# Kernel tuning notes

Hardware: AMD Instinct MI355X
Metric: run time of the kernel (lower is better)

The kernel has to match this reference:

```python
import jax, jax.numpy as jnp
import numpy as np

N_NODES = 10000
N_EDGES = 640000
DIM = 128


def setup_inputs() -> dict:
    key = jax.random.key(0)
    ks = jax.random.split(key, 10)
    s = 1.0 / np.sqrt(DIM)
    return {
        "x": jax.random.normal(ks[0], (N_NODES, DIM), dtype=jnp.float32),
        "edge_index": jax.random.randint(ks[1], (2, N_EDGES), 0, N_NODES, dtype=jnp.int64),
        "fc_w": jax.random.normal(ks[2], (DIM, DIM), dtype=jnp.float32) * s,
        "fc_b": jax.random.normal(ks[3], (DIM,), dtype=jnp.float32) * s,
        "f_lw": jax.random.normal(ks[4], (DIM, DIM), dtype=jnp.float32) * s,
        "f_lb": jax.random.normal(ks[5], (DIM,), dtype=jnp.float32) * s,
        "f_rw": jax.random.normal(ks[6], (DIM, DIM), dtype=jnp.float32) * s,
        "n_lw": jax.random.normal(ks[7], (DIM, DIM), dtype=jnp.float32) * s,
        "n_lb": jax.random.normal(ks[8], (DIM,), dtype=jnp.float32) * s,
        "n_rw": jax.random.normal(ks[9], (DIM, DIM), dtype=jnp.float32) * s,
    }


def _sage_conv(h, src, dst, lw, lb, rw, n_nodes):
    # mean aggregation of source-node features at target nodes
    msg = h[src]                                                   # [E, D]
    summed = jax.ops.segment_sum(msg, dst, num_segments=n_nodes)   # [N, D]
    cnt = jax.ops.segment_sum(jnp.ones_like(dst, dtype=h.dtype), dst, num_segments=n_nodes)
    agg = summed / jnp.maximum(cnt, 1.0)[:, None]
    # PyG SAGEConv: lin_l(agg) + lin_r(x); lin_l has bias, lin_r does not
    return agg @ lw.T + lb + h @ rw.T


def reference(x, edge_index, fc_w, fc_b, f_lw, f_lb, f_rw, n_lw, n_lb, n_rw):
    n_nodes = x.shape[0]
    src, dst = edge_index[0], edge_index[1]
    inp = x @ fc_w.T + fc_b                                        # fc residual branch
    h = jax.nn.relu(_sage_conv(x, src, dst, f_lw, f_lb, f_rw, n_nodes))
    # dropout(p=0.3) is identity in eval mode
    h = _sage_conv(h, src, dst, n_lw, n_lb, n_rw, n_nodes)
    return jax.nn.relu(h + inp)
```

## Files before the change

### kernel.cpp

```cpp
#include <hip/hip_runtime.h>

#define NN 10000
#define NE 640000
#define DIM 128
#define NB 157
#define REGCAP 4608
#define MT1 157
#define G_FILL 625
#define NODECAP 128

typedef __attribute__((ext_vector_type(8))) short bf16x8;
typedef __attribute__((ext_vector_type(4))) float f32x4;

__device__ __forceinline__ unsigned short f2bf(float f) {
    unsigned u = __float_as_uint(f);
    u += 0x7FFFu + ((u >> 16) & 1u);
    return (unsigned short)(u >> 16);
}
__device__ __forceinline__ float bf2f(unsigned short h) {
    return __uint_as_float(((unsigned)h) << 16);
}

__global__ __launch_bounds__(256) void prep_k(
        const float* __restrict__ w0, const float* __restrict__ w1,
        const float* __restrict__ w2, const float* __restrict__ w3,
        const float* __restrict__ w4,
        unsigned short* __restrict__ wb, int* __restrict__ gcur) {
    int t = blockIdx.x * 256 + threadIdx.x;
    if (t < NB) gcur[t] = t * REGCAP;
    int plane = t >> 14;
    int i = t & 16383;
    const float* wp = (plane == 0) ? w0 : (plane == 1) ? w1 :
                      (plane == 2) ? w2 : (plane == 3) ? w3 : w4;
    wb[t] = f2bf(wp[i]);
}

__global__ __launch_bounds__(256) void mega1_k(
        const float* __restrict__ A,
        const unsigned short* __restrict__ wb,
        unsigned short* __restrict__ xlb,
        float* __restrict__ xr, float* __restrict__ xc,
        const int* __restrict__ src, const int* __restrict__ dst,
        int* __restrict__ gcur, unsigned* __restrict__ region) {
    int b = blockIdx.x;
    int tid = threadIdx.x;
    if (b < G_FILL) {
        __shared__ int start[NB + 1];
        __shared__ int cur[NB];
        __shared__ int gbase[NB];
        __shared__ unsigned sorted[1024];
        if (tid < NB + 1) start[tid] = 0;
        __syncthreads();
        int e4 = b * 1024 + tid * 4;
        int4 s = *(const int4*)(src + e4);
        int4 d = *(const int4*)(dst + e4);
        unsigned p0 = ((unsigned)d.x << 16) | (unsigned)s.x;
        unsigned p1 = ((unsigned)d.y << 16) | (unsigned)s.y;
        unsigned p2 = ((unsigned)d.z << 16) | (unsigned)s.z;
        unsigned p3 = ((unsigned)d.w << 16) | (unsigned)s.w;
        int k0 = d.x >> 6, k1 = d.y >> 6, k2 = d.z >> 6, k3 = d.w >> 6;
        atomicAdd(&start[k0 + 1], 1);
        atomicAdd(&start[k1 + 1], 1);
        atomicAdd(&start[k2 + 1], 1);
        atomicAdd(&start[k3 + 1], 1);
        __syncthreads();
        for (int off = 1; off < NB + 1; off <<= 1) {
            int v = 0;
            if (tid <= NB && tid >= off) v = start[tid - off];
            __syncthreads();
            if (tid <= NB && tid >= off) start[tid] += v;
            __syncthreads();
        }
        if (tid < NB) cur[tid] = start[tid];
        __syncthreads();
        int q;
        q = atomicAdd(&cur[k0], 1); sorted[q] = p0;
        q = atomicAdd(&cur[k1], 1); sorted[q] = p1;
        q = atomicAdd(&cur[k2], 1); sorted[q] = p2;
        q = atomicAdd(&cur[k3], 1); sorted[q] = p3;
        __syncthreads();
        if (tid < NB) {
            int len = start[tid + 1] - start[tid];
            gbase[tid] = (len > 0) ? atomicAdd(&gcur[tid], len) : 0;
        }
        __syncthreads();
#pragma unroll
        for (int i = tid; i < 1024; i += 256) {
            unsigned e = sorted[i];
            int bb = (int)(e >> 16) >> 6;
            int gpos = gbase[bb] + (i - start[bb]);
            if (gpos < (bb + 1) * REGCAP) region[gpos] = e;
        }
        return;
    }
    int gb = b - G_FILL;
    int plane = gb / MT1;
    int mt = gb % MT1;
    const unsigned short* W = wb + (size_t)plane * (DIM * DIM);
    int lane = tid & 63;
    int wv = tid >> 6;
    int mr = lane & 15, q = lane >> 4;
    int m0 = mt * 64 + wv * 16;
    int mc = min(m0 + mr, NN - 1);

    bf16x8 afr[4];
#pragma unroll
    for (int kc = 0; kc < 4; ++kc) {
        const float* ap = A + (size_t)mc * DIM + kc * 32 + q * 8;
        float4 v0 = *(const float4*)ap;
        float4 v1 = *(const float4*)(ap + 4);
        bf16x8 f;
        f[0] = (short)f2bf(v0.x); f[1] = (short)f2bf(v0.y);
        f[2] = (short)f2bf(v0.z); f[3] = (short)f2bf(v0.w);
        f[4] = (short)f2bf(v1.x); f[5] = (short)f2bf(v1.y);
        f[6] = (short)f2bf(v1.z); f[7] = (short)f2bf(v1.w);
        afr[kc] = f;
    }
    f32x4 acc[8];
#pragma unroll
    for (int nt = 0; nt < 8; ++nt) acc[nt] = (f32x4){0.f, 0.f, 0.f, 0.f};
#pragma unroll
    for (int nt = 0; nt < 8; ++nt) {
        const unsigned short* wp = W + (size_t)(nt * 16 + mr) * DIM;
#pragma unroll
        for (int kc = 0; kc < 4; ++kc) {
            bf16x8 wfr = *(const bf16x8*)(const void*)(wp + kc * 32 + q * 8);
            acc[nt] = __builtin_amdgcn_mfma_f32_16x16x32_bf16(afr[kc], wfr, acc[nt], 0, 0, 0);
        }
    }
#pragma unroll
    for (int r = 0; r < 4; ++r) {
        int ms = m0 + q * 4 + r;
        if (ms >= NN) continue;
        if (plane == 0) {
#pragma unroll
            for (int nt = 0; nt < 8; ++nt)
                xlb[(size_t)ms * DIM + nt * 16 + mr] = f2bf(acc[nt][r]);
        } else {
            float* o = (plane == 1) ? xr : xc;
#pragma unroll
            for (int nt = 0; nt < 8; ++nt)
                o[(size_t)ms * DIM + nt * 16 + mr] = acc[nt][r];
        }
    }
}

template<int MODE>
__global__ __launch_bounds__(256) void agg_k(
        const unsigned short* __restrict__ gsrc,
        const float* __restrict__ xr, const float* __restrict__ b0v,
        const int* __restrict__ gcur, const unsigned* __restrict__ region,
        unsigned short* __restrict__ outb) {
    int blk = blockIdx.x;
    int b = blk >> 2, sub = blk & 3;
    int n0 = b * 64 + sub * 16;
    int tid = threadIdx.x;
    __shared__ unsigned short list[16][NODECAP];
    __shared__ int cnt[16];
    if (tid < 16) cnt[tid] = 0;
    __syncthreads();
    int R = min(gcur[b] - b * REGCAP, REGCAP);
    const unsigned* reg = region + (size_t)b * REGCAP;
    for (int i = tid; i < R; i += 256) {
        unsigned e = reg[i];
        int nl = (int)(e >> 16) - n0;
        if ((unsigned)nl < 16u) {
            int slot = atomicAdd(&cnt[nl], 1);
            if (slot < NODECAP) list[nl][slot] = (unsigned short)(e & 0xFFFFu);
        }
    }
    __syncthreads();

    int g = tid >> 4, d8 = tid & 15;
    int node = n0 + g;
    if (node >= NN) return;
    int deg = min(cnt[g], NODECAP);
    float a[8];
#pragma unroll
    for (int j = 0; j < 8; ++j) a[j] = 0.f;
    union U { int4 v; unsigned short us[8]; };
    int r = 0;
    for (; r + 4 <= deg; r += 4) {
        int i0 = list[g][r + 0];
        int i1 = list[g][r + 1];
        int i2 = list[g][r + 2];
        int i3 = list[g][r + 3];
        U u0, u1, u2, u3;
        u0.v = *(const int4*)(const void*)(gsrc + (size_t)i0 * DIM + d8 * 8);
        u1.v = *(const int4*)(const void*)(gsrc + (size_t)i1 * DIM + d8 * 8);
        u2.v = *(const int4*)(const void*)(gsrc + (size_t)i2 * DIM + d8 * 8);
        u3.v = *(const int4*)(const void*)(gsrc + (size_t)i3 * DIM + d8 * 8);
#pragma unroll
        for (int j = 0; j < 8; ++j)
            a[j] += bf2f(u0.us[j]) + bf2f(u1.us[j]) + bf2f(u2.us[j]) + bf2f(u3.us[j]);
    }
    for (; r < deg; ++r) {
        int i0 = list[g][r];
        U u0;
        u0.v = *(const int4*)(const void*)(gsrc + (size_t)i0 * DIM + d8 * 8);
#pragma unroll
        for (int j = 0; j < 8; ++j) a[j] += bf2f(u0.us[j]);
    }
    float inv = 1.f / fmaxf((float)deg, 1.f);
    U o;
    if (MODE == 0) {
        const float* xp = xr + (size_t)node * DIM + d8 * 8;
        float4 r0 = *(const float4*)xp;
        float4 r1 = *(const float4*)(xp + 4);
        const float* bp = b0v + d8 * 8;
        float4 c0 = *(const float4*)bp;
        float4 c1 = *(const float4*)(bp + 4);
        float rv[8] = {r0.x, r0.y, r0.z, r0.w, r1.x, r1.y, r1.z, r1.w};
        float bv[8] = {c0.x, c0.y, c0.z, c0.w, c1.x, c1.y, c1.z, c1.w};
#pragma unroll
        for (int j = 0; j < 8; ++j)
            o.us[j] = f2bf(fmaxf(a[j] * inv + rv[j] + bv[j], 0.f));
    } else {
#pragma unroll
        for (int j = 0; j < 8; ++j) o.us[j] = f2bf(a[j] * inv);
    }
    *(int4*)(void*)(outb + (size_t)node * DIM + d8 * 8) = o.v;
}

__global__ __launch_bounds__(256) void mega2_k(
        const unsigned short* __restrict__ m1b,
        const unsigned short* __restrict__ h1b,
        const unsigned short* __restrict__ wb,
        const float* __restrict__ xc,
        const float* __restrict__ nlb, const float* __restrict__ fcb,
        float* __restrict__ out) {
    const unsigned short* W0 = wb + (size_t)3 * DIM * DIM;
    const unsigned short* W1 = wb + (size_t)4 * DIM * DIM;
    int lane = threadIdx.x & 63;
    int wv = threadIdx.x >> 6;
    int mr = lane & 15, q = lane >> 4;
    int m0 = (int)blockIdx.x * 64 + wv * 16;
    int mc = min(m0 + mr, NN - 1);

    bf16x8 a0[4], a1[4];
#pragma unroll
    for (int kc = 0; kc < 4; ++kc) {
        a0[kc] = *(const bf16x8*)(const void*)(m1b + (size_t)mc * DIM + kc * 32 + q * 8);
        a1[kc] = *(const bf16x8*)(const void*)(h1b + (size_t)mc * DIM + kc * 32 + q * 8);
    }
    f32x4 acc[8];
#pragma unroll
    for (int nt = 0; nt < 8; ++nt) acc[nt] = (f32x4){0.f, 0.f, 0.f, 0.f};
#pragma unroll
    for (int nt = 0; nt < 8; ++nt) {
        const unsigned short* w0p = W0 + (size_t)(nt * 16 + mr) * DIM;
        const unsigned short* w1p = W1 + (size_t)(nt * 16 + mr) * DIM;
#pragma unroll
        for (int kc = 0; kc < 4; ++kc) {
            bf16x8 wf0 = *(const bf16x8*)(const void*)(w0p + kc * 32 + q * 8);
            acc[nt] = __builtin_amdgcn_mfma_f32_16x16x32_bf16(a0[kc], wf0, acc[nt], 0, 0, 0);
            bf16x8 wf1 = *(const bf16x8*)(const void*)(w1p + kc * 32 + q * 8);
            acc[nt] = __builtin_amdgcn_mfma_f32_16x16x32_bf16(a1[kc], wf1, acc[nt], 0, 0, 0);
        }
    }
    float bias[8];
#pragma unroll
    for (int nt = 0; nt < 8; ++nt) {
        int col = nt * 16 + mr;
        bias[nt] = nlb[col] + fcb[col];
    }
#pragma unroll
    for (int r = 0; r < 4; ++r) {
        int ms = m0 + q * 4 + r;
        if (ms >= NN) continue;
#pragma unroll
        for (int nt = 0; nt < 8; ++nt) {
            int col = nt * 16 + mr;
            float v = acc[nt][r] + xc[(size_t)ms * DIM + col] + bias[nt];
            out[(size_t)ms * DIM + col] = fmaxf(v, 0.f);
        }
    }
}

extern "C" void kernel_launch(void* const* d_in, const int* in_sizes, int n_in,
                              void* d_out, int out_size, void* d_ws, size_t ws_size,
                              hipStream_t stream) {
    const float* x    = (const float*)d_in[0];
    const int*   edge = (const int*)d_in[1];
    const float* fc_w = (const float*)d_in[2];
    const float* fc_b = (const float*)d_in[3];
    const float* f_lw = (const float*)d_in[4];
    const float* f_lb = (const float*)d_in[5];
    const float* f_rw = (const float*)d_in[6];
    const float* n_lw = (const float*)d_in[7];
    const float* n_lb = (const float*)d_in[8];
    const float* n_rw = (const float*)d_in[9];
    float* out = (float*)d_out;

    const int* src = edge;
    const int* dst = edge + NE;

    char* p = (char*)d_ws;
    float* xr = (float*)p;                     p += (size_t)NN * DIM * sizeof(float);
    float* xc = (float*)p;                     p += (size_t)NN * DIM * sizeof(float);
    unsigned short* xlb = (unsigned short*)p;  p += (size_t)NN * DIM * sizeof(unsigned short);
    unsigned short* h1b = (unsigned short*)p;  p += (size_t)NN * DIM * sizeof(unsigned short);
    unsigned short* m1b = (unsigned short*)p;  p += (size_t)NN * DIM * sizeof(unsigned short);
    unsigned short* wb  = (unsigned short*)p;  p += (size_t)5 * DIM * DIM * sizeof(unsigned short);
    int* gcur = (int*)p;                       p += (size_t)256 * sizeof(int);
    unsigned* region = (unsigned*)p;

    prep_k<<<(5 * DIM * DIM) / 256, 256, 0, stream>>>(f_lw, f_rw, fc_w, n_lw, n_rw, wb, gcur);
    mega1_k<<<G_FILL + 3 * MT1, 256, 0, stream>>>(
        x, wb, xlb, xr, xc, src, dst, gcur, region);
    agg_k<0><<<4 * NB, 256, 0, stream>>>(xlb, xr, f_lb, gcur, region, h1b);
    agg_k<1><<<4 * NB, 256, 0, stream>>>(h1b, nullptr, nullptr, gcur, region, m1b);
    mega2_k<<<MT1, 256, 0, stream>>>(m1b, h1b, wb, xc, n_lb, fc_b, out);
}
```

Measured before the change: 152.3 us.

## Fuse second aggregation into final GEMM and drop weight prep kernel

Removes the weight-conversion prep kernel: weights are now converted from fp32 to bf16 on the fly inside the GEMM kernels, and gcur is zeroed with a memset instead. The second mean aggregation is fused into the final GEMM kernel, with the aggregated features staged in shared memory rather than written to and re-read from a global buffer. This cuts launches and global traffic, but the fused kernel runs only 157 blocks that do all aggregation work, and every block now re-reads the fp32 weights. The gather loop is also unrolled from 4 to 8 loads, and the mean now divides by the true degree rather than the capped one.

```diff
diff --git a/kernel.cpp b/kernel.cpp
--- a/kernel.cpp
+++ b/kernel.cpp
@@ -20,24 +20,21 @@
 __device__ __forceinline__ float bf2f(unsigned short h) {
     return __uint_as_float(((unsigned)h) << 16);
 }
-
-__global__ __launch_bounds__(256) void prep_k(
-        const float* __restrict__ w0, const float* __restrict__ w1,
-        const float* __restrict__ w2, const float* __restrict__ w3,
-        const float* __restrict__ w4,
-        unsigned short* __restrict__ wb, int* __restrict__ gcur) {
-    int t = blockIdx.x * 256 + threadIdx.x;
-    if (t < NB) gcur[t] = t * REGCAP;
-    int plane = t >> 14;
-    int i = t & 16383;
-    const float* wp = (plane == 0) ? w0 : (plane == 1) ? w1 :
-                      (plane == 2) ? w2 : (plane == 3) ? w3 : w4;
-    wb[t] = f2bf(wp[i]);
+__device__ __forceinline__ bf16x8 ldw8(const float* p) {
+    float4 v0 = *(const float4*)p;
+    float4 v1 = *(const float4*)(p + 4);
+    bf16x8 f;
+    f[0] = (short)f2bf(v0.x); f[1] = (short)f2bf(v0.y);
+    f[2] = (short)f2bf(v0.z); f[3] = (short)f2bf(v0.w);
+    f[4] = (short)f2bf(v1.x); f[5] = (short)f2bf(v1.y);
+    f[6] = (short)f2bf(v1.z); f[7] = (short)f2bf(v1.w);
+    return f;
 }
 
 __global__ __launch_bounds__(256) void mega1_k(
         const float* __restrict__ A,
-        const unsigned short* __restrict__ wb,
+        const float* __restrict__ W0f, const float* __restrict__ W1f,
+        const float* __restrict__ W2f,
         unsigned short* __restrict__ xlb,
         float* __restrict__ xr, float* __restrict__ xc,
         const int* __restrict__ src, const int* __restrict__ dst,
@@ -88,15 +85,15 @@
         for (int i = tid; i < 1024; i += 256) {
             unsigned e = sorted[i];
             int bb = (int)(e >> 16) >> 6;
-            int gpos = gbase[bb] + (i - start[bb]);
-            if (gpos < (bb + 1) * REGCAP) region[gpos] = e;
+            int rel = gbase[bb] + (i - start[bb]);
+            if (rel < REGCAP) region[(size_t)bb * REGCAP + rel] = e;
         }
         return;
     }
     int gb = b - G_FILL;
     int plane = gb / MT1;
     int mt = gb % MT1;
-    const unsigned short* W = wb + (size_t)plane * (DIM * DIM);
+    const float* W = (plane == 0) ? W0f : ((plane == 1) ? W1f : W2f);
     int lane = tid & 63;
     int wv = tid >> 6;
     int mr = lane & 15, q = lane >> 4;
@@ -105,26 +102,17 @@
 
     bf16x8 afr[4];
 #pragma unroll
-    for (int kc = 0; kc < 4; ++kc) {
-        const float* ap = A + (size_t)mc * DIM + kc * 32 + q * 8;
-        float4 v0 = *(const float4*)ap;
-        float4 v1 = *(const float4*)(ap + 4);
-        bf16x8 f;
-        f[0] = (short)f2bf(v0.x); f[1] = (short)f2bf(v0.y);
-        f[2] = (short)f2bf(v0.z); f[3] = (short)f2bf(v0.w);
-        f[4] = (short)f2bf(v1.x); f[5] = (short)f2bf(v1.y);
-        f[6] = (short)f2bf(v1.z); f[7] = (short)f2bf(v1.w);
-        afr[kc] = f;
-    }
+    for (int kc = 0; kc < 4; ++kc)
+        afr[kc] = ldw8(A + (size_t)mc * DIM + kc * 32 + q * 8);
     f32x4 acc[8];
 #pragma unroll
     for (int nt = 0; nt < 8; ++nt) acc[nt] = (f32x4){0.f, 0.f, 0.f, 0.f};
 #pragma unroll
     for (int nt = 0; nt < 8; ++nt) {
-        const unsigned short* wp = W + (size_t)(nt * 16 + mr) * DIM;
+        const float* wp = W + (size_t)(nt * 16 + mr) * DIM;
 #pragma unroll
         for (int kc = 0; kc < 4; ++kc) {
-            bf16x8 wfr = *(const bf16x8*)(const void*)(wp + kc * 32 + q * 8);
+            bf16x8 wfr = ldw8(wp + kc * 32 + q * 8);
             acc[nt] = __builtin_amdgcn_mfma_f32_16x16x32_bf16(afr[kc], wfr, acc[nt], 0, 0, 0);
         }
     }
@@ -145,8 +133,7 @@
     }
 }
 
-template<int MODE>
-__global__ __launch_bounds__(256) void agg_k(
+__global__ __launch_bounds__(256) void agg1_k(
         const unsigned short* __restrict__ gsrc,
         const float* __restrict__ xr, const float* __restrict__ b0v,
         const int* __restrict__ gcur, const unsigned* __restrict__ region,
@@ -159,7 +146,7 @@
     __shared__ int cnt[16];
     if (tid < 16) cnt[tid] = 0;
     __syncthreads();
-    int R = min(gcur[b] - b * REGCAP, REGCAP);
+    int R = min(gcur[b], REGCAP);
     const unsigned* reg = region + (size_t)b * REGCAP;
     for (int i = tid; i < R; i += 256) {
         unsigned e = reg[i];
@@ -174,25 +161,24 @@
     int g = tid >> 4, d8 = tid & 15;
     int node = n0 + g;
     if (node >= NN) return;
-    int deg = min(cnt[g], NODECAP);
+    int trueDeg = cnt[g];
+    int deg = min(trueDeg, NODECAP);
     float a[8];
 #pragma unroll
     for (int j = 0; j < 8; ++j) a[j] = 0.f;
     union U { int4 v; unsigned short us[8]; };
     int r = 0;
-    for (; r + 4 <= deg; r += 4) {
-        int i0 = list[g][r + 0];
-        int i1 = list[g][r + 1];
-        int i2 = list[g][r + 2];
-        int i3 = list[g][r + 3];
-        U u0, u1, u2, u3;
-        u0.v = *(const int4*)(const void*)(gsrc + (size_t)i0 * DIM + d8 * 8);
-        u1.v = *(const int4*)(const void*)(gsrc + (size_t)i1 * DIM + d8 * 8);
-        u2.v = *(const int4*)(const void*)(gsrc + (size_t)i2 * DIM + d8 * 8);
-        u3.v = *(const int4*)(const void*)(gsrc + (size_t)i3 * DIM + d8 * 8);
-#pragma unroll
-        for (int j = 0; j < 8; ++j)
-            a[j] += bf2f(u0.us[j]) + bf2f(u1.us[j]) + bf2f(u2.us[j]) + bf2f(u3.us[j]);
+    for (; r + 8 <= deg; r += 8) {
+        U u[8];
+#pragma unroll
+        for (int t = 0; t < 8; ++t) {
+            int i0 = list[g][r + t];
+            u[t].v = *(const int4*)(const void*)(gsrc + (size_t)i0 * DIM + d8 * 8);
+        }
+#pragma unroll
+        for (int t = 0; t < 8; ++t)
+#pragma unroll
+            for (int j = 0; j < 8; ++j) a[j] += bf2f(u[t].us[j]);
     }
     for (; r < deg; ++r) {
         int i0 = list[g][r];
@@ -201,46 +187,101 @@
 #pragma unroll
         for (int j = 0; j < 8; ++j) a[j] += bf2f(u0.us[j]);
     }
-    float inv = 1.f / fmaxf((float)deg, 1.f);
+    float inv = 1.f / fmaxf((float)trueDeg, 1.f);
+    const float* xp = xr + (size_t)node * DIM + d8 * 8;
+    float4 r0 = *(const float4*)xp;
+    float4 r1 = *(const float4*)(xp + 4);
+    const float* bp = b0v + d8 * 8;
+    float4 c0 = *(const float4*)bp;
+    float4 c1 = *(const float4*)(bp + 4);
+    float rv[8] = {r0.x, r0.y, r0.z, r0.w, r1.x, r1.y, r1.z, r1.w};
+    float bv[8] = {c0.x, c0.y, c0.z, c0.w, c1.x, c1.y, c1.z, c1.w};
     U o;
-    if (MODE == 0) {
-        const float* xp = xr + (size_t)node * DIM + d8 * 8;
-        float4 r0 = *(const float4*)xp;
-        float4 r1 = *(const float4*)(xp + 4);
-        const float* bp = b0v + d8 * 8;
-        float4 c0 = *(const float4*)bp;
-        float4 c1 = *(const float4*)(bp + 4);
-        float rv[8] = {r0.x, r0.y, r0.z, r0.w, r1.x, r1.y, r1.z, r1.w};
-        float bv[8] = {c0.x, c0.y, c0.z, c0.w, c1.x, c1.y, c1.z, c1.w};
-#pragma unroll
-        for (int j = 0; j < 8; ++j)
-            o.us[j] = f2bf(fmaxf(a[j] * inv + rv[j] + bv[j], 0.f));
-    } else {
-#pragma unroll
-        for (int j = 0; j < 8; ++j) o.us[j] = f2bf(a[j] * inv);
-    }
+#pragma unroll
+    for (int j = 0; j < 8; ++j)
+        o.us[j] = f2bf(fmaxf(a[j] * inv + rv[j] + bv[j], 0.f));
     *(int4*)(void*)(outb + (size_t)node * DIM + d8 * 8) = o.v;
 }
 
-__global__ __launch_bounds__(256) void mega2_k(
-        const unsigned short* __restrict__ m1b,
+__global__ __launch_bounds__(256) void k3_k(
         const unsigned short* __restrict__ h1b,
-        const unsigned short* __restrict__ wb,
+        const float* __restrict__ nlw, const float* __restrict__ nrw,
         const float* __restrict__ xc,
         const float* __restrict__ nlb, const float* __restrict__ fcb,
+        const int* __restrict__ gcur, const unsigned* __restrict__ region,
         float* __restrict__ out) {
-    const unsigned short* W0 = wb + (size_t)3 * DIM * DIM;
-    const unsigned short* W1 = wb + (size_t)4 * DIM * DIM;
-    int lane = threadIdx.x & 63;
-    int wv = threadIdx.x >> 6;
+    int b = blockIdx.x;
+    int tid = threadIdx.x;
+    __shared__ unsigned short list[64][NODECAP];
+    __shared__ int cnt[64];
+    __shared__ unsigned short m1[64][136];
+    if (tid < 64) cnt[tid] = 0;
+    __syncthreads();
+    int n0 = b * 64;
+    int R = min(gcur[b], REGCAP);
+    const unsigned* reg = region + (size_t)b * REGCAP;
+    for (int i = tid; i < R; i += 256) {
+        unsigned e = reg[i];
+        int nl = (int)(e >> 16) - n0;
+        int slot = atomicAdd(&cnt[nl], 1);
+        if (slot < NODECAP) list[nl][slot] = (unsigned short)(e & 0xFFFFu);
+    }
+    __syncthreads();
+
+    int g = tid >> 4, d8 = tid & 15;
+    union U { int4 v; unsigned short us[8]; };
+#pragma unroll
+    for (int sub = 0; sub < 4; ++sub) {
+        int nl = sub * 16 + g;
+        int node = n0 + nl;
+        float a[8];
+#pragma unroll
+        for (int j = 0; j < 8; ++j) a[j] = 0.f;
+        if (node < NN) {
+            int trueDeg = cnt[nl];
+            int deg = min(trueDeg, NODECAP);
+            int r = 0;
+            for (; r + 8 <= deg; r += 8) {
+                U u[8];
+#pragma unroll
+                for (int t = 0; t < 8; ++t) {
+                    int i0 = list[nl][r + t];
+                    u[t].v = *(const int4*)(const void*)(h1b + (size_t)i0 * DIM + d8 * 8);
+                }
+#pragma unroll
+                for (int t = 0; t < 8; ++t)
+#pragma unroll
+                    for (int j = 0; j < 8; ++j) a[j] += bf2f(u[t].us[j]);
+            }
+            for (; r < deg; ++r) {
+                int i0 = list[nl][r];
+                U u0;
+                u0.v = *(const int4*)(const void*)(h1b + (size_t)i0 * DIM + d8 * 8);
+#pragma unroll
+                for (int j = 0; j < 8; ++j) a[j] += bf2f(u0.us[j]);
+            }
+            float inv = 1.f / fmaxf((float)trueDeg, 1.f);
+#pragma unroll
+            for (int j = 0; j < 8; ++j) a[j] *= inv;
+        }
+        U o;
+#pragma unroll
+        for (int j = 0; j < 8; ++j) o.us[j] = f2bf(a[j]);
+        *(int4*)(void*)&m1[nl][d8 * 8] = o.v;
+    }
+    __syncthreads();
+
+    int lane = tid & 63;
+    int wv = tid >> 6;
     int mr = lane & 15, q = lane >> 4;
-    int m0 = (int)blockIdx.x * 64 + wv * 16;
+    int m0 = n0 + wv * 16;
+    int ml = wv * 16 + mr;
     int mc = min(m0 + mr, NN - 1);
 
     bf16x8 a0[4], a1[4];
 #pragma unroll
     for (int kc = 0; kc < 4; ++kc) {
-        a0[kc] = *(const bf16x8*)(const void*)(m1b + (size_t)mc * DIM + kc * 32 + q * 8);
+        a0[kc] = *(const bf16x8*)(const void*)&m1[ml][kc * 32 + q * 8];
         a1[kc] = *(const bf16x8*)(const void*)(h1b + (size_t)mc * DIM + kc * 32 + q * 8);
     }
     f32x4 acc[8];
@@ -248,13 +289,13 @@
     for (int nt = 0; nt < 8; ++nt) acc[nt] = (f32x4){0.f, 0.f, 0.f, 0.f};
 #pragma unroll
     for (int nt = 0; nt < 8; ++nt) {
-        const unsigned short* w0p = W0 + (size_t)(nt * 16 + mr) * DIM;
-        const unsigned short* w1p = W1 + (size_t)(nt * 16 + mr) * DIM;
+        const float* w0p = nlw + (size_t)(nt * 16 + mr) * DIM;
+        const float* w1p = nrw + (size_t)(nt * 16 + mr) * DIM;
 #pragma unroll
         for (int kc = 0; kc < 4; ++kc) {
-            bf16x8 wf0 = *(const bf16x8*)(const void*)(w0p + kc * 32 + q * 8);
+            bf16x8 wf0 = ldw8(w0p + kc * 32 + q * 8);
             acc[nt] = __builtin_amdgcn_mfma_f32_16x16x32_bf16(a0[kc], wf0, acc[nt], 0, 0, 0);
-            bf16x8 wf1 = *(const bf16x8*)(const void*)(w1p + kc * 32 + q * 8);
+            bf16x8 wf1 = ldw8(w1p + kc * 32 + q * 8);
             acc[nt] = __builtin_amdgcn_mfma_f32_16x16x32_bf16(a1[kc], wf1, acc[nt], 0, 0, 0);
         }
     }
@@ -300,15 +341,12 @@
     float* xc = (float*)p;                     p += (size_t)NN * DIM * sizeof(float);
     unsigned short* xlb = (unsigned short*)p;  p += (size_t)NN * DIM * sizeof(unsigned short);
     unsigned short* h1b = (unsigned short*)p;  p += (size_t)NN * DIM * sizeof(unsigned short);
-    unsigned short* m1b = (unsigned short*)p;  p += (size_t)NN * DIM * sizeof(unsigned short);
-    unsigned short* wb  = (unsigned short*)p;  p += (size_t)5 * DIM * DIM * sizeof(unsigned short);
     int* gcur = (int*)p;                       p += (size_t)256 * sizeof(int);
     unsigned* region = (unsigned*)p;
 
-    prep_k<<<(5 * DIM * DIM) / 256, 256, 0, stream>>>(f_lw, f_rw, fc_w, n_lw, n_rw, wb, gcur);
+    hipMemsetAsync(gcur, 0, 256 * sizeof(int), stream);
     mega1_k<<<G_FILL + 3 * MT1, 256, 0, stream>>>(
-        x, wb, xlb, xr, xc, src, dst, gcur, region);
-    agg_k<0><<<4 * NB, 256, 0, stream>>>(xlb, xr, f_lb, gcur, region, h1b);
-    agg_k<1><<<4 * NB, 256, 0, stream>>>(h1b, nullptr, nullptr, gcur, region, m1b);
-    mega2_k<<<MT1, 256, 0, stream>>>(m1b, h1b, wb, xc, n_lb, fc_b, out);
-}
+        x, f_lw, f_rw, fc_w, xlb, xr, xc, src, dst, gcur, region);
+    agg1_k<<<4 * NB, 256, 0, stream>>>(xlb, xr, f_lb, gcur, region, h1b);
+    k3_k<<<NB, 256, 0, stream>>>(h1b, n_lw, n_rw, xc, n_lb, fc_b, gcur, region, out);
+}
```

Result: slower. 178.7 us (+17.3%).

## Store gathered node features in FP8 e4m3 for neighbor aggregation

Applied to the files above, without the earlier changes.

The per-node features that the aggregation kernels gather (the projected input and the first-layer hidden state) are now stored as FP8 e4m3 rather than bf16, which halves the bytes read per neighbor row. The gather loop is unrolled to eight neighbors at a time. The first aggregation kernel writes both a bf16 and an FP8 copy of its hidden output, and the region cursor becomes a relative count. The mean now divides by the true degree instead of the capped one. The cost is a large loss of precision in the aggregated sums, which risks failing the accuracy tolerance.

```diff
diff --git a/kernel.cpp b/kernel.cpp
--- a/kernel.cpp
+++ b/kernel.cpp
@@ -1,4 +1,5 @@
 #include <hip/hip_runtime.h>
+#include <hip/hip_fp8.h>
 
 #define NN 10000
 #define NE 640000
@@ -20,6 +21,15 @@
 __device__ __forceinline__ float bf2f(unsigned short h) {
     return __uint_as_float(((unsigned)h) << 16);
 }
+__device__ __forceinline__ unsigned char f2f8(float f) {
+    __hip_fp8_e4m3 t(f);
+    return (unsigned char)t.__x;
+}
+__device__ __forceinline__ float f82f(unsigned char u) {
+    __hip_fp8_e4m3 t;
+    t.__x = (__hip_fp8_storage_t)u;
+    return (float)t;
+}
 
 __global__ __launch_bounds__(256) void prep_k(
         const float* __restrict__ w0, const float* __restrict__ w1,
@@ -27,7 +37,7 @@
         const float* __restrict__ w4,
         unsigned short* __restrict__ wb, int* __restrict__ gcur) {
     int t = blockIdx.x * 256 + threadIdx.x;
-    if (t < NB) gcur[t] = t * REGCAP;
+    if (t < 256) gcur[t] = 0;
     int plane = t >> 14;
     int i = t & 16383;
     const float* wp = (plane == 0) ? w0 : (plane == 1) ? w1 :
@@ -38,7 +48,7 @@
 __global__ __launch_bounds__(256) void mega1_k(
         const float* __restrict__ A,
         const unsigned short* __restrict__ wb,
-        unsigned short* __restrict__ xlb,
+        unsigned char* __restrict__ xl8,
         float* __restrict__ xr, float* __restrict__ xc,
         const int* __restrict__ src, const int* __restrict__ dst,
         int* __restrict__ gcur, unsigned* __restrict__ region) {
@@ -88,8 +98,8 @@
         for (int i = tid; i < 1024; i += 256) {
             unsigned e = sorted[i];
             int bb = (int)(e >> 16) >> 6;
-            int gpos = gbase[bb] + (i - start[bb]);
-            if (gpos < (bb + 1) * REGCAP) region[gpos] = e;
+            int rel = gbase[bb] + (i - start[bb]);
+            if (rel < REGCAP) region[(size_t)bb * REGCAP + rel] = e;
         }
         return;
     }
@@ -135,7 +145,7 @@
         if (plane == 0) {
 #pragma unroll
             for (int nt = 0; nt < 8; ++nt)
-                xlb[(size_t)ms * DIM + nt * 16 + mr] = f2bf(acc[nt][r]);
+                xl8[(size_t)ms * DIM + nt * 16 + mr] = f2f8(acc[nt][r]);
         } else {
             float* o = (plane == 1) ? xr : xc;
 #pragma unroll
@@ -147,10 +157,10 @@
 
 template<int MODE>
 __global__ __launch_bounds__(256) void agg_k(
-        const unsigned short* __restrict__ gsrc,
+        const unsigned char* __restrict__ g8,
         const float* __restrict__ xr, const float* __restrict__ b0v,
         const int* __restrict__ gcur, const unsigned* __restrict__ region,
-        unsigned short* __restrict__ outb) {
+        unsigned short* __restrict__ outb, unsigned char* __restrict__ out8) {
     int blk = blockIdx.x;
     int b = blk >> 2, sub = blk & 3;
     int n0 = b * 64 + sub * 16;
@@ -159,7 +169,7 @@
     __shared__ int cnt[16];
     if (tid < 16) cnt[tid] = 0;
     __syncthreads();
-    int R = min(gcur[b] - b * REGCAP, REGCAP);
+    int R = min(gcur[b], REGCAP);
     const unsigned* reg = region + (size_t)b * REGCAP;
     for (int i = tid; i < R; i += 256) {
         unsigned e = reg[i];
@@ -174,35 +184,34 @@
     int g = tid >> 4, d8 = tid & 15;
     int node = n0 + g;
     if (node >= NN) return;
-    int deg = min(cnt[g], NODECAP);
+    int trueDeg = cnt[g];
+    int deg = min(trueDeg, NODECAP);
     float a[8];
 #pragma unroll
     for (int j = 0; j < 8; ++j) a[j] = 0.f;
-    union U { int4 v; unsigned short us[8]; };
+    union U { uint2 v; unsigned char c[8]; };
     int r = 0;
-    for (; r + 4 <= deg; r += 4) {
-        int i0 = list[g][r + 0];
-        int i1 = list[g][r + 1];
-        int i2 = list[g][r + 2];
-        int i3 = list[g][r + 3];
-        U u0, u1, u2, u3;
-        u0.v = *(const int4*)(const void*)(gsrc + (size_t)i0 * DIM + d8 * 8);
-        u1.v = *(const int4*)(const void*)(gsrc + (size_t)i1 * DIM + d8 * 8);
-        u2.v = *(const int4*)(const void*)(gsrc + (size_t)i2 * DIM + d8 * 8);
-        u3.v = *(const int4*)(const void*)(gsrc + (size_t)i3 * DIM + d8 * 8);
-#pragma unroll
-        for (int j = 0; j < 8; ++j)
-            a[j] += bf2f(u0.us[j]) + bf2f(u1.us[j]) + bf2f(u2.us[j]) + bf2f(u3.us[j]);
+    for (; r + 8 <= deg; r += 8) {
+        U u[8];
+#pragma unroll
+        for (int t = 0; t < 8; ++t) {
+            int i0 = list[g][r + t];
+            u[t].v = *(const uint2*)(const void*)(g8 + (size_t)i0 * DIM + d8 * 8);
+        }
+#pragma unroll
+        for (int t = 0; t < 8; ++t)
+#pragma unroll
+            for (int j = 0; j < 8; ++j) a[j] += f82f(u[t].c[j]);
     }
     for (; r < deg; ++r) {
         int i0 = list[g][r];
         U u0;
-        u0.v = *(const int4*)(const void*)(gsrc + (size_t)i0 * DIM + d8 * 8);
-#pragma unroll
-        for (int j = 0; j < 8; ++j) a[j] += bf2f(u0.us[j]);
-    }
-    float inv = 1.f / fmaxf((float)deg, 1.f);
-    U o;
+        u0.v = *(const uint2*)(const void*)(g8 + (size_t)i0 * DIM + d8 * 8);
+#pragma unroll
+        for (int j = 0; j < 8; ++j) a[j] += f82f(u0.c[j]);
+    }
+    float inv = 1.f / fmaxf((float)trueDeg, 1.f);
+    union B { int4 v; unsigned short us[8]; } o;
     if (MODE == 0) {
         const float* xp = xr + (size_t)node * DIM + d8 * 8;
         float4 r0 = *(const float4*)xp;
@@ -212,14 +221,20 @@
         float4 c1 = *(const float4*)(bp + 4);
         float rv[8] = {r0.x, r0.y, r0.z, r0.w, r1.x, r1.y, r1.z, r1.w};
         float bv[8] = {c0.x, c0.y, c0.z, c0.w, c1.x, c1.y, c1.z, c1.w};
-#pragma unroll
-        for (int j = 0; j < 8; ++j)
-            o.us[j] = f2bf(fmaxf(a[j] * inv + rv[j] + bv[j], 0.f));
+        U o8;
+#pragma unroll
+        for (int j = 0; j < 8; ++j) {
+            float v = fmaxf(a[j] * inv + rv[j] + bv[j], 0.f);
+            o.us[j] = f2bf(v);
+            o8.c[j] = f2f8(v);
+        }
+        *(int4*)(void*)(outb + (size_t)node * DIM + d8 * 8) = o.v;
+        *(uint2*)(void*)(out8 + (size_t)node * DIM + d8 * 8) = o8.v;
     } else {
 #pragma unroll
         for (int j = 0; j < 8; ++j) o.us[j] = f2bf(a[j] * inv);
-    }
-    *(int4*)(void*)(outb + (size_t)node * DIM + d8 * 8) = o.v;
+        *(int4*)(void*)(outb + (size_t)node * DIM + d8 * 8) = o.v;
+    }
 }
 
 __global__ __launch_bounds__(256) void mega2_k(
@@ -298,17 +313,18 @@
     char* p = (char*)d_ws;
     float* xr = (float*)p;                     p += (size_t)NN * DIM * sizeof(float);
     float* xc = (float*)p;                     p += (size_t)NN * DIM * sizeof(float);
-    unsigned short* xlb = (unsigned short*)p;  p += (size_t)NN * DIM * sizeof(unsigned short);
     unsigned short* h1b = (unsigned short*)p;  p += (size_t)NN * DIM * sizeof(unsigned short);
     unsigned short* m1b = (unsigned short*)p;  p += (size_t)NN * DIM * sizeof(unsigned short);
     unsigned short* wb  = (unsigned short*)p;  p += (size_t)5 * DIM * DIM * sizeof(unsigned short);
+    unsigned char* xl8  = (unsigned char*)p;   p += (size_t)NN * DIM;
+    unsigned char* h18  = (unsigned char*)p;   p += (size_t)NN * DIM;
     int* gcur = (int*)p;                       p += (size_t)256 * sizeof(int);
     unsigned* region = (unsigned*)p;
 
     prep_k<<<(5 * DIM * DIM) / 256, 256, 0, stream>>>(f_lw, f_rw, fc_w, n_lw, n_rw, wb, gcur);
     mega1_k<<<G_FILL + 3 * MT1, 256, 0, stream>>>(
-        x, wb, xlb, xr, xc, src, dst, gcur, region);
-    agg_k<0><<<4 * NB, 256, 0, stream>>>(xlb, xr, f_lb, gcur, region, h1b);
-    agg_k<1><<<4 * NB, 256, 0, stream>>>(h1b, nullptr, nullptr, gcur, region, m1b);
+        x, wb, xl8, xr, xc, src, dst, gcur, region);
+    agg_k<0><<<4 * NB, 256, 0, stream>>>(xl8, xr, f_lb, gcur, region, h1b, h18);
+    agg_k<1><<<4 * NB, 256, 0, stream>>>(h18, nullptr, nullptr, gcur, region, m1b, nullptr);
     mega2_k<<<MT1, 256, 0, stream>>>(m1b, h1b, wb, xc, n_lb, fc_b, out);
 }
```

Measured after the change: 155.0 us. Within noise of the previous version (+1.8%).
